# Performance work log

Measured on AMD Instinct MI355X. Metric: run time of the kernel, lower is better.

The kernel has to match this reference:

```python
import jax, jax.numpy as jnp
import numpy as np

B, N, T, D = 64, 76, 128, 128
AH, HEADS, DFF, FAH = 8, 4, 512, 128
DK = D // HEADS


def layer_norm(x, a, b, eps=1e-7):
    mean = x.mean(-1, keepdims=True)
    std = jnp.std(x, -1, ddof=1, keepdims=True)  # torch.std is unbiased
    return a * (x - mean) / (std + eps) + b


def setup_inputs() -> dict:
    key = jax.random.key(0)
    ks = jax.random.split(key, 32)
    w = lambda i, shape, s=0.05: (jax.random.normal(ks[i], shape, jnp.float32) * s)
    return {
        "H": jax.random.normal(ks[0], (B, N, T, D), jnp.float32),
        "mask": jax.random.randint(ks[1], (B, N, T), 0, 2).astype(jnp.float32),
        "feature_mask": jax.random.uniform(ks[2], (B, N), dtype=jnp.float32),
        # MissingAwareTemporalAttention params (shared across features)
        "Wt": w(3, (D, AH), 0.1), "Wx": w(4, (D, AH), 0.1),
        "rate": jnp.array([0.8], jnp.float32),
        "obs_bias": jnp.float32(0.5), "miss_bias": jnp.float32(0.0),
        # MultiHeadedAttention params (weights stored [in,out])
        "Wq": w(5, (D, D)), "bq": jnp.zeros(D, jnp.float32),
        "Wk": w(6, (D, D)), "bk": jnp.zeros(D, jnp.float32),
        "Wv": w(7, (D, D)), "bv": jnp.zeros(D, jnp.float32),
        "Wo": w(8, (D, D)), "bo": jnp.zeros(D, jnp.float32),
        # SublayerConnection LayerNorms
        "ln1_a": jnp.ones(D, jnp.float32), "ln1_b": jnp.zeros(D, jnp.float32),
        "ln2_a": jnp.ones(D, jnp.float32), "ln2_b": jnp.zeros(D, jnp.float32),
        # PositionwiseFeedForward
        "w1": w(9, (D, DFF)), "b1": jnp.zeros(DFF, jnp.float32),
        "w2": w(10, (DFF, D)), "b2": jnp.zeros(D, jnp.float32),
        # FinalAttentionQKV ('mul')
        "fWq": w(11, (D, FAH)), "fbq": jnp.zeros(FAH, jnp.float32),
        "fWk": w(12, (D, FAH)), "fbk": jnp.zeros(FAH, jnp.float32),
        "fWv": w(13, (D, FAH)), "fbv": jnp.zeros(FAH, jnp.float32),
        "mask_scale": jnp.float32(1.0),
    }


def concare_forward(H, mask, feature_mask, Wt, Wx, rate, obs_bias, miss_bias,
                    Wq, bq, Wk, bk, Wv, bv, Wo, bo, ln1_a, ln1_b, ln2_a, ln2_b,
                    w1, b1, w2, b2, fWq, fbq, fWk, fbk, fWv, fbv, mask_scale):
    # ---- MissingAwareTemporalAttention per feature (vectorized over N) ----
    q = jnp.einsum('bnd,da->bna', H[:, :, -1, :], Wt)           # [B,N,AH]
    k = jnp.einsum('bntd,da->bnta', H, Wx)                      # [B,N,T,AH]
    dot = jnp.einsum('bna,bnta->bnt', q, k)                     # [B,N,T]
    b_time = (jnp.arange(T - 1, -1, -1, dtype=jnp.float32) + 1.0)  # [T]
    sig = jax.nn.sigmoid(dot)
    denom = jax.nn.sigmoid(rate[0]) * (jnp.log(2.72 + (1.0 - sig)) * b_time)
    e = jax.nn.relu(sig / denom)
    e = e + jnp.where(mask > 0.5, obs_bias, miss_bias)
    a = jax.nn.softmax(e, axis=-1)                              # over T
    emb = jnp.einsum('bnt,bntd->bnd', a, H)                     # [B,N,D]

    # ---- SublayerConnection 1: pre-norm + MultiHeadedAttention + residual ----
    x0 = layer_norm(emb, ln1_a, ln1_b)
    qh = (x0 @ Wq + bq).reshape(B, N, HEADS, DK).transpose(0, 2, 1, 3)
    kh = (x0 @ Wk + bk).reshape(B, N, HEADS, DK).transpose(0, 2, 1, 3)
    vh = (x0 @ Wv + bv).reshape(B, N, HEADS, DK).transpose(0, 2, 1, 3)
    scores = jnp.einsum('bhqd,bhkd->bhqk', qh, kh) / np.sqrt(DK)
    p = jax.nn.softmax(scores, axis=-1)
    ctx = jnp.einsum('bhqk,bhkd->bhqd', p, vh).transpose(0, 2, 1, 3).reshape(B, N, D)
    mha = ctx @ Wo + bo                                          # [B,N,D]
    # DeCov regularizer over batch, per feature position
    feats = jnp.transpose(mha, (1, 2, 0))                        # [N,D,B]
    centered = feats - feats.mean(axis=2, keepdims=True)
    cov = jnp.einsum('ndb,neb->nde', centered, centered) / (B - 1)
    diag = jnp.einsum('ndd->nd', cov)
    decov = 0.5 * (jnp.sum(cov ** 2) - jnp.sum(diag ** 2))
    x = emb + mha

    # ---- SublayerConnection 2: pre-norm + FFN + residual ----
    x1 = layer_norm(x, ln2_a, ln2_b)
    ffn = jax.nn.relu(x1 @ w1 + b1) @ w2 + b2
    x = x + ffn                                                  # [B,N,D]

    # ---- FinalAttentionQKV ('mul') ----
    fq = x[:, -1, :] @ fWq + fbq                                 # [B,FAH]
    fk = x @ fWk + fbk                                           # [B,N,FAH]
    fv = x @ fWv + fbv                                           # [B,N,FAH]
    fe = jnp.einsum('bna,ba->bn', fk, fq)
    fe = fe + mask_scale * feature_mask
    alpha = jax.nn.softmax(fe, axis=1)                           # over N
    pooled = jnp.einsum('bn,bna->ba', alpha, fv)                 # [B,FAH]
    return pooled, decov


def reference(H, mask, feature_mask, Wt, Wx, rate, obs_bias, miss_bias,
              Wq, bq, Wk, bk, Wv, bv, Wo, bo, ln1_a, ln1_b, ln2_a, ln2_b,
              w1, b1, w2, b2, fWq, fbq, fWk, fbk, fWv, fbv, mask_scale):
    return concare_forward(H, mask, feature_mask, Wt, Wx, rate, obs_bias, miss_bias,
                           Wq, bq, Wk, bk, Wv, bv, Wo, bo, ln1_a, ln1_b, ln2_a, ln2_b,
                           w1, b1, w2, b2, fWq, fbq, fWk, fbk, fWv, fbv, mask_scale)
```

## Files before the change

kernel.cpp:

```cpp
#include <hip/hip_runtime.h>
#include <hip/hip_bf16.h>
#include <math.h>

#define BB 64
#define NN 76
#define TT 128
#define DD 128
#define AH 8
#define NHEADS 4
#define DFF 512
#define FAH 128
#define DK 32
#define BN (BB*NN)
#define ROWS 8
#define NBLK (BN/ROWS)

__device__ __forceinline__ void bar_lds() {
    asm volatile("s_waitcnt lgkmcnt(0)" ::: "memory");
    __builtin_amdgcn_s_barrier();
    __builtin_amdgcn_sched_barrier(0);
}

__global__ __launch_bounds__(512, 6) void k1_temporal(
    const float* __restrict__ H, const float* __restrict__ mask,
    const float* __restrict__ Wt, const float* __restrict__ Wx,
    const float* __restrict__ rate, const float* __restrict__ obs_bias,
    const float* __restrict__ miss_bias, float* __restrict__ emb)
{
    __shared__ __align__(16) float wqs[DD];
    __shared__ __align__(16) float dots[TT];
    __shared__ __align__(16) float as_[TT];
    __shared__ __align__(16) float parts[16][DD];
    __shared__ float qpart[2][AH];
    __shared__ float redmax[2];
    __shared__ float redsum[2];

    const int bid = blockIdx.x;
    const int tid = threadIdx.x;
    const size_t base = (size_t)bid * (TT*DD);

    float r127 = 0.f, maskv = 0.f;
    float4 wt0 = {0,0,0,0}, wt1 = {0,0,0,0}, wx0 = {0,0,0,0}, wx1 = {0,0,0,0};
    if (tid < DD) {
        r127 = H[base + (TT-1)*DD + tid];
        wt0 = *(const float4*)&Wt[tid*AH + 0];
        wt1 = *(const float4*)&Wt[tid*AH + 4];
        wx0 = *(const float4*)&Wx[tid*AH + 0];
        wx1 = *(const float4*)&Wx[tid*AH + 4];
        maskv = mask[(size_t)bid*TT + tid];
    }
    const float ratev = rate[0], obsv = obs_bias[0], missv = miss_bias[0];

    float4 h[8];
    const float4* Hg4 = (const float4*)(H + base);
    #pragma unroll
    for (int j = 0; j < 8; ++j) h[j] = Hg4[j*512 + tid];

    if (tid < DD) {
        float p[AH] = {r127*wt0.x, r127*wt0.y, r127*wt0.z, r127*wt0.w,
                       r127*wt1.x, r127*wt1.y, r127*wt1.z, r127*wt1.w};
        #pragma unroll
        for (int a = 0; a < AH; ++a) {
            float v = p[a];
            #pragma unroll
            for (int m = 1; m < 64; m <<= 1) v += __shfl_xor(v, m, 64);
            if ((tid & 63) == 0) qpart[tid >> 6][a] = v;
        }
    }
    bar_lds();
    if (tid < DD) {
        const float q0 = qpart[0][0]+qpart[1][0], q1 = qpart[0][1]+qpart[1][1];
        const float q2 = qpart[0][2]+qpart[1][2], q3 = qpart[0][3]+qpart[1][3];
        const float q4 = qpart[0][4]+qpart[1][4], q5 = qpart[0][5]+qpart[1][5];
        const float q6 = qpart[0][6]+qpart[1][6], q7 = qpart[0][7]+qpart[1][7];
        wqs[tid] = q0*wx0.x + q1*wx0.y + q2*wx0.z + q3*wx0.w
                 + q4*wx1.x + q5*wx1.y + q6*wx1.z + q7*wx1.w;
    }
    bar_lds();

    const int c = tid & 31, g = tid >> 5;
    const float4 wq4 = *(const float4*)&wqs[4*c];
    #pragma unroll
    for (int j = 0; j < 8; ++j) {
        float p = h[j].x*wq4.x + h[j].y*wq4.y + h[j].z*wq4.z + h[j].w*wq4.w;
        #pragma unroll
        for (int m = 1; m < 32; m <<= 1) p += __shfl_xor(p, m, 64);
        if (c == 0) dots[g + 16*j] = p;
    }
    bar_lds();

    const int lane = tid & 63, w = tid >> 6;
    float ev = -1e30f;
    if (tid < TT) {
        const float dot = dots[tid];
        const float sig = 1.f / (1.f + expf(-dot));
        const float sr  = 1.f / (1.f + expf(-ratev));
        const float bt  = (float)(TT - tid);
        const float denom = sr * (logf(2.72f + (1.f - sig)) * bt);
        float e = fmaxf(sig / denom, 0.f);
        e += (maskv > 0.5f) ? obsv : missv;
        ev = e;
        float vmax = ev;
        #pragma unroll
        for (int m = 1; m < 64; m <<= 1) vmax = fmaxf(vmax, __shfl_xor(vmax, m, 64));
        if (lane == 0) redmax[w] = vmax;
    }
    bar_lds();
    const float mx = fmaxf(redmax[0], redmax[1]);
    const float ex = (tid < TT) ? expf(ev - mx) : 0.f;
    if (tid < TT) {
        float vs = ex;
        #pragma unroll
        for (int m = 1; m < 64; m <<= 1) vs += __shfl_xor(vs, m, 64);
        if (lane == 0) redsum[w] = vs;
    }
    bar_lds();
    const float ssum = redsum[0] + redsum[1];
    if (tid < TT) as_[tid] = ex / ssum;
    bar_lds();

    float4 facc = make_float4(0.f, 0.f, 0.f, 0.f);
    #pragma unroll
    for (int j = 0; j < 8; ++j) {
        const float a = as_[g + 16*j];
        facc.x += a*h[j].x; facc.y += a*h[j].y;
        facc.z += a*h[j].z; facc.w += a*h[j].w;
    }
    *(float4*)&parts[g][4*c] = facc;
    bar_lds();
    if (tid < DD) {
        float acc = 0.f;
        #pragma unroll
        for (int gg = 0; gg < 16; ++gg) acc += parts[gg][tid];
        emb[(size_t)bid*DD + tid] = acc;
    }
}

__global__ __launch_bounds__(256) void k2a_ln_qkv(
    const float* __restrict__ emb,
    const float* __restrict__ ln_a, const float* __restrict__ ln_b,
    const float* __restrict__ Wq, const float* __restrict__ bq,
    const float* __restrict__ Wk, const float* __restrict__ bk,
    const float* __restrict__ Wv, const float* __restrict__ bv,
    float* __restrict__ qb, float* __restrict__ kb, float* __restrict__ vb)
{
    __shared__ float xs[ROWS][DD];
    const int tid = threadIdx.x;
    const int r0 = blockIdx.x * ROWS;

    for (int i = tid; i < ROWS*DD; i += 256) {
        const int r = i / DD, d = i % DD;
        xs[r][d] = emb[(size_t)(r0+r)*DD + d];
    }
    __syncthreads();

    {
        const int wv_ = tid >> 6, lane = tid & 63;
        for (int rr = 0; rr < 2; ++rr) {
            const int r = wv_*2 + rr;
            const float x0 = xs[r][lane], x1 = xs[r][lane+64];
            float s = x0 + x1;
            #pragma unroll
            for (int m = 1; m < 64; m <<= 1) s += __shfl_xor(s, m, 64);
            const float mean = s / (float)DD;
            const float d0 = x0 - mean, d1 = x1 - mean;
            float v = d0*d0 + d1*d1;
            #pragma unroll
            for (int m = 1; m < 64; m <<= 1) v += __shfl_xor(v, m, 64);
            const float inv = 1.f / (sqrtf(v / (float)(DD-1)) + 1e-7f);
            xs[r][lane]    = ln_a[lane]   * (d0*inv) + ln_b[lane];
            xs[r][lane+64] = ln_a[lane+64]* (d1*inv) + ln_b[lane+64];
        }
    }
    __syncthreads();

    const int j = tid & 127, half = tid >> 7, rbase = half*4;
    float aq[4] = {0,0,0,0}, ak[4] = {0,0,0,0}, av[4] = {0,0,0,0};
    for (int d = 0; d < DD; ++d) {
        const float wqv = Wq[d*DD+j], wkv = Wk[d*DD+j], wvv = Wv[d*DD+j];
        #pragma unroll
        for (int r = 0; r < 4; ++r) {
            const float xv = xs[rbase+r][d];
            aq[r] += xv*wqv; ak[r] += xv*wkv; av[r] += xv*wvv;
        }
    }
    const float bqv = bq[j], bkv = bk[j], bvv = bv[j];
    #pragma unroll
    for (int r = 0; r < 4; ++r) {
        const size_t o = (size_t)(r0 + rbase + r)*DD + j;
        qb[o] = aq[r]+bqv; kb[o] = ak[r]+bkv; vb[o] = av[r]+bvv;
    }
}

__global__ __launch_bounds__(128) void k2b_attn(
    const float* __restrict__ qb, const float* __restrict__ kb,
    const float* __restrict__ vb, float* __restrict__ ctx)
{
    __shared__ float Qs[NN][DK], Ks[NN][DK], Vs[NN][DK];
    __shared__ float Ps[NN][NN+1];
    const int b = blockIdx.x / NHEADS, h = blockIdx.x % NHEADS;
    const int tid = threadIdx.x;
    const int co = h*DK;

    for (int i = tid; i < NN*DK; i += 128) {
        const int r = i / DK, c = i % DK;
        const size_t o = (size_t)(b*NN + r)*DD + co + c;
        Qs[r][c] = qb[o]; Ks[r][c] = kb[o]; Vs[r][c] = vb[o];
    }
    __syncthreads();

    const float scale = 0.17677669529663687f;
    if (tid < NN) {
        float qr[DK];
        #pragma unroll
        for (int c = 0; c < DK; ++c) qr[c] = Qs[tid][c];
        float mx = -1e30f;
        for (int k = 0; k < NN; ++k) {
            float s = 0.f;
            #pragma unroll
            for (int c = 0; c < DK; ++c) s += qr[c]*Ks[k][c];
            s *= scale;
            Ps[tid][k] = s;
            mx = fmaxf(mx, s);
        }
        float sum = 0.f;
        for (int k = 0; k < NN; ++k) { const float e = expf(Ps[tid][k]-mx); Ps[tid][k] = e; sum += e; }
        const float inv = 1.f/sum;
        float acc[DK];
        #pragma unroll
        for (int c = 0; c < DK; ++c) acc[c] = 0.f;
        for (int k = 0; k < NN; ++k) {
            const float p = Ps[tid][k];
            #pragma unroll
            for (int c = 0; c < DK; ++c) acc[c] += p*Vs[k][c];
        }
        const size_t o = (size_t)(b*NN + tid)*DD + co;
        #pragma unroll
        for (int c = 0; c < DK; ++c) ctx[o+c] = acc[c]*inv;
    }
}

__global__ __launch_bounds__(256) void k23_proj_ffn(
    const float* __restrict__ ctx, const float* __restrict__ emb,
    const float* __restrict__ Wo, const float* __restrict__ bo,
    const float* __restrict__ ln_a, const float* __restrict__ ln_b,
    const float* __restrict__ w1, const float* __restrict__ b1,
    const float* __restrict__ w2, const float* __restrict__ b2,
    float* __restrict__ mha, float* __restrict__ x2)
{
    __shared__ float cs[ROWS][DD];
    __shared__ float xs[ROWS][DD];
    __shared__ float x1s[ROWS][DD];
    __shared__ float hs[ROWS][DFF];
    __shared__ float parts[2][ROWS][DD];
    const int tid = threadIdx.x;
    const int r0 = blockIdx.x * ROWS;

    for (int i = tid; i < ROWS*DD; i += 256) {
        const int r = i / DD, d = i % DD;
        cs[r][d] = ctx[(size_t)(r0+r)*DD + d];
    }
    __syncthreads();

    {
        const int j = tid & 127, half = tid >> 7, rbase = half*4;
        float acc[4] = {0,0,0,0};
        for (int d = 0; d < DD; ++d) {
            const float wv = Wo[d*DD+j];
            #pragma unroll
            for (int r = 0; r < 4; ++r) acc[r] += cs[rbase+r][d]*wv;
        }
        const float bov = bo[j];
        #pragma unroll
        for (int r = 0; r < 4; ++r) {
            const size_t o = (size_t)(r0+rbase+r)*DD + j;
            const float m = acc[r] + bov;
            mha[o] = m;
            xs[rbase+r][j] = emb[o] + m;
        }
    }
    __syncthreads();

    {
        const int wv_ = tid >> 6, lane = tid & 63;
        for (int rr = 0; rr < 2; ++rr) {
            const int r = wv_*2 + rr;
            const float v0 = xs[r][lane], v1 = xs[r][lane+64];
            float s = v0 + v1;
            #pragma unroll
            for (int m = 1; m < 64; m <<= 1) s += __shfl_xor(s, m, 64);
            const float mean = s / (float)DD;
            const float d0 = v0-mean, d1 = v1-mean;
            float vv = d0*d0 + d1*d1;
            #pragma unroll
            for (int m = 1; m < 64; m <<= 1) vv += __shfl_xor(vv, m, 64);
            const float inv = 1.f / (sqrtf(vv/(float)(DD-1)) + 1e-7f);
            x1s[r][lane]    = ln_a[lane]   * (d0*inv) + ln_b[lane];
            x1s[r][lane+64] = ln_a[lane+64]* (d1*inv) + ln_b[lane+64];
        }
    }
    __syncthreads();

    {
        float acc0[ROWS], acc1[ROWS];
        #pragma unroll
        for (int r = 0; r < ROWS; ++r) { acc0[r]=0.f; acc1[r]=0.f; }
        for (int d = 0; d < DD; ++d) {
            const float wv0 = w1[d*DFF + tid], wv1 = w1[d*DFF + tid + 256];
            #pragma unroll
            for (int r = 0; r < ROWS; ++r) {
                const float xv = x1s[r][d];
                acc0[r] += xv*wv0; acc1[r] += xv*wv1;
            }
        }
        const float b10 = b1[tid], b11 = b1[tid+256];
        #pragma unroll
        for (int r = 0; r < ROWS; ++r) {
            hs[r][tid]     = fmaxf(acc0[r]+b10, 0.f);
            hs[r][tid+256] = fmaxf(acc1[r]+b11, 0.f);
        }
    }
    __syncthreads();

    {
        const int j = tid & 127, half = tid >> 7;
        float acc[ROWS];
        #pragma unroll
        for (int r = 0; r < ROWS; ++r) acc[r] = 0.f;
        for (int k = half*256; k < half*256 + 256; ++k) {
            const float wv = w2[k*DD + j];
            #pragma unroll
            for (int r = 0; r < ROWS; ++r) acc[r] += hs[r][k]*wv;
        }
        #pragma unroll
        for (int r = 0; r < ROWS; ++r) parts[half][r][j] = acc[r];
        __syncthreads();
        if (half == 0) {
            const float b2v = b2[j];
            #pragma unroll
            for (int r = 0; r < ROWS; ++r) {
                const size_t o = (size_t)(r0+r)*DD + j;
                x2[o] = xs[r][j] + parts[0][r][j] + parts[1][r][j] + b2v;
            }
        }
    }
}

__global__ __launch_bounds__(256) void k_decov(
    const float* __restrict__ mha, float* __restrict__ partial)
{
    __shared__ float Cs[BB][DD];
    __shared__ float means[DD];
    __shared__ float reda[256];
    __shared__ float redb[256];
    const int n = blockIdx.x, dc = blockIdx.y;
    const int tid = threadIdx.x;
    for (int i = tid; i < BB*DD; i += 256) {
        const int bb = i / DD, d = i % DD;
        Cs[bb][d] = mha[((size_t)bb*NN + n)*DD + d];
    }
    __syncthreads();
    if (tid < DD) {
        float s = 0.f;
        for (int bb = 0; bb < BB; ++bb) s += Cs[bb][tid];
        means[tid] = s / (float)BB;
    }
    __syncthreads();
    if (tid < DD) {
        const float m = means[tid];
        for (int bb = 0; bb < BB; ++bb) Cs[bb][tid] -= m;
    }
    __syncthreads();
    float ss = 0.f, dd2 = 0.f;
    const float invB1 = 1.f/63.f;
    for (int qi = tid; qi < 1024; qi += 256) {
        const int d  = dc*32 + qi / 32;
        const int e4 = (qi % 32) * 4;
        float a0=0,a1=0,a2=0,a3=0;
        for (int bb = 0; bb < BB; ++bb) {
            const float cd = Cs[bb][d];
            const float4 ce = *(const float4*)&Cs[bb][e4];
            a0 += cd*ce.x; a1 += cd*ce.y; a2 += cd*ce.z; a3 += cd*ce.w;
        }
        a0*=invB1; a1*=invB1; a2*=invB1; a3*=invB1;
        ss += a0*a0+a1*a1+a2*a2+a3*a3;
        if (d >= e4 && d < e4+4) {
            const float c[4] = {a0,a1,a2,a3};
            const float cd = c[d-e4];
            dd2 += cd*cd;
        }
    }
    reda[tid] = ss; redb[tid] = dd2;
    __syncthreads();
    for (int s2 = 128; s2 >= 1; s2 >>= 1) {
        if (tid < s2) { reda[tid] += reda[tid+s2]; redb[tid] += redb[tid+s2]; }
        __syncthreads();
    }
    if (tid == 0) partial[n*4 + dc] = 0.5f*(reda[0] - redb[0]);
}

__global__ __launch_bounds__(128) void k4_final(
    const float* __restrict__ x, const float* __restrict__ feature_mask,
    const float* __restrict__ fWq, const float* __restrict__ fbq,
    const float* __restrict__ fWk, const float* __restrict__ fbk,
    const float* __restrict__ fWv, const float* __restrict__ fbv,
    const float* __restrict__ mask_scale, const float* __restrict__ decov_partial,
    float* __restrict__ out)
{
    __shared__ float Xs[NN][DD];
    __shared__ float fqs[DD], gs[DD], ys[DD];
    __shared__ float es[NN];
    __shared__ float sc[2];
    const int b = blockIdx.x;
    const int tid = threadIdx.x;
    for (int i = tid; i < NN*DD; i += 128) {
        const int r = i / DD, d = i % DD;
        Xs[r][d] = x[((size_t)b*NN + r)*DD + d];
    }
    __syncthreads();
    {
        float acc = 0.f;
        for (int d = 0; d < DD; ++d) acc += Xs[NN-1][d] * fWq[d*FAH + tid];
        fqs[tid] = acc + fbq[tid];
    }
    __syncthreads();
    {
        float acc = 0.f;
        for (int a = 0; a < FAH; ++a) acc += fWk[tid*FAH + a] * fqs[a];
        gs[tid] = acc;
    }
    if (tid == 0) {
        float acc = 0.f;
        for (int a = 0; a < FAH; ++a) acc += fbk[a]*fqs[a];
        sc[0] = acc;
    }
    __syncthreads();
    const float msc = mask_scale[0];
    if (tid < NN) {
        float acc = 0.f;
        for (int d = 0; d < DD; ++d) acc += Xs[tid][d]*gs[d];
        es[tid] = acc + sc[0] + msc * feature_mask[b*NN + tid];
    }
    __syncthreads();
    if (tid == 0) {
        float mx = -1e30f;
        for (int n2 = 0; n2 < NN; ++n2) mx = fmaxf(mx, es[n2]);
        float sum = 0.f;
        for (int n2 = 0; n2 < NN; ++n2) { const float e = expf(es[n2]-mx); es[n2] = e; sum += e; }
        sc[1] = 1.f/sum;
    }
    __syncthreads();
    {
        const float inv = sc[1];
        float acc = 0.f;
        for (int n2 = 0; n2 < NN; ++n2) acc += es[n2]*Xs[n2][tid];
        ys[tid] = acc * inv;
    }
    __syncthreads();
    {
        float acc = 0.f;
        for (int d = 0; d < DD; ++d) acc += ys[d]*fWv[d*FAH + tid];
        out[(size_t)b*FAH + tid] = acc + fbv[tid];
    }
    if (b == 0 && tid == 0) {
        float s = 0.f;
        for (int i = 0; i < NN*4; ++i) s += decov_partial[i];
        out[BB*FAH] = s;
    }
}

extern "C" void kernel_launch(void* const* d_in, const int* in_sizes, int n_in,
                              void* d_out, int out_size, void* d_ws, size_t ws_size,
                              hipStream_t stream) {
    const float* H    = (const float*)d_in[0];
    const float* mask = (const float*)d_in[1];
    const float* fm   = (const float*)d_in[2];
    const float* Wt   = (const float*)d_in[3];
    const float* Wx   = (const float*)d_in[4];
    const float* rate = (const float*)d_in[5];
    const float* obs_bias  = (const float*)d_in[6];
    const float* miss_bias = (const float*)d_in[7];
    const float* Wq = (const float*)d_in[8];   const float* bq = (const float*)d_in[9];
    const float* Wk = (const float*)d_in[10];  const float* bk = (const float*)d_in[11];
    const float* Wv = (const float*)d_in[12];  const float* bv = (const float*)d_in[13];
    const float* Wo = (const float*)d_in[14];  const float* bo = (const float*)d_in[15];
    const float* ln1a = (const float*)d_in[16]; const float* ln1b = (const float*)d_in[17];
    const float* ln2a = (const float*)d_in[18]; const float* ln2b = (const float*)d_in[19];
    const float* w1 = (const float*)d_in[20];  const float* b1 = (const float*)d_in[21];
    const float* w2 = (const float*)d_in[22];  const float* b2 = (const float*)d_in[23];
    const float* fWq = (const float*)d_in[24]; const float* fbq = (const float*)d_in[25];
    const float* fWk = (const float*)d_in[26]; const float* fbk = (const float*)d_in[27];
    const float* fWv = (const float*)d_in[28]; const float* fbv = (const float*)d_in[29];
    const float* mask_scale = (const float*)d_in[30];
    float* out = (float*)d_out;

    float* ws = (float*)d_ws;
    const size_t S = (size_t)BN*DD;
    float* emb = ws;
    float* qb  = ws + 1*S;
    float* kb  = ws + 2*S;
    float* vb  = ws + 3*S;
    float* ctx = ws + 4*S;
    float* mha = ws + 5*S;
    float* x2  = ws + 6*S;
    float* dpart = ws + 7*S;

    k1_temporal<<<BN, 512, 0, stream>>>(H, mask, Wt, Wx, rate, obs_bias, miss_bias, emb);
    k2a_ln_qkv<<<NBLK, 256, 0, stream>>>(emb, ln1a, ln1b, Wq, bq, Wk, bk, Wv, bv, qb, kb, vb);
    k2b_attn<<<BB*NHEADS, 128, 0, stream>>>(qb, kb, vb, ctx);
    k23_proj_ffn<<<NBLK, 256, 0, stream>>>(ctx, emb, Wo, bo, ln2a, ln2b, w1, b1, w2, b2, mha, x2);
    k_decov<<<dim3(NN, 4), 256, 0, stream>>>(mha, dpart);
    k4_final<<<BB, 128, 0, stream>>>(x2, fm, fWq, fbq, fWk, fbk, fWv, fbv, mask_scale, dpart, out);
}
```

Measured before the change: 181.3 us.

## Make temporal kernel persistent with double-buffered LDS DMA prefetch of H tiles

The temporal attention kernel becomes persistent: 256 blocks each loop over 19 (b,n) sequences instead of one block per sequence. Each 64KB H tile is copied straight into LDS with global_load_lds, double-buffered so the next tile loads while the current one is processed. This aims to hide HBM latency and cut launch and scheduling overhead. The cost is 128KB of LDS per block (one block per CU), a single tile of lookahead, and two redundant tile loads per block at the loop tail.

```diff
diff --git a/kernel.cpp b/kernel.cpp
--- a/kernel.cpp
+++ b/kernel.cpp
@@ -14,6 +14,8 @@
 #define BN (BB*NN)
 #define ROWS 8
 #define NBLK (BN/ROWS)
+#define K1BLK 256
+#define K1NT (BN/K1BLK)
 
 __device__ __forceinline__ void bar_lds() {
     asm volatile("s_waitcnt lgkmcnt(0)" ::: "memory");
@@ -21,12 +23,19 @@
     __builtin_amdgcn_sched_barrier(0);
 }
 
-__global__ __launch_bounds__(512, 6) void k1_temporal(
+__device__ __forceinline__ void dma16(const float* g, float* l) {
+    __builtin_amdgcn_global_load_lds(
+        (__attribute__((address_space(1))) void*)g,
+        (__attribute__((address_space(3))) void*)l, 16, 0, 0);
+}
+
+__global__ __launch_bounds__(512) void k1_temporal(
     const float* __restrict__ H, const float* __restrict__ mask,
     const float* __restrict__ Wt, const float* __restrict__ Wx,
     const float* __restrict__ rate, const float* __restrict__ obs_bias,
     const float* __restrict__ miss_bias, float* __restrict__ emb)
 {
+    __shared__ __align__(16) float buf[2][TT*DD];
     __shared__ __align__(16) float wqs[DD];
     __shared__ __align__(16) float dots[TT];
     __shared__ __align__(16) float as_[TT];
@@ -35,104 +44,137 @@
     __shared__ float redmax[2];
     __shared__ float redsum[2];
 
-    const int bid = blockIdx.x;
     const int tid = threadIdx.x;
-    const size_t base = (size_t)bid * (TT*DD);
-
-    float r127 = 0.f, maskv = 0.f;
+    const int lane = tid & 63, w = tid >> 6;
+    const int c = tid & 31, g = tid >> 5;
+    const int t0 = blockIdx.x * K1NT;
+
     float4 wt0 = {0,0,0,0}, wt1 = {0,0,0,0}, wx0 = {0,0,0,0}, wx1 = {0,0,0,0};
+    float mA = 0.f, mB = 0.f;
     if (tid < DD) {
-        r127 = H[base + (TT-1)*DD + tid];
         wt0 = *(const float4*)&Wt[tid*AH + 0];
         wt1 = *(const float4*)&Wt[tid*AH + 4];
         wx0 = *(const float4*)&Wx[tid*AH + 0];
         wx1 = *(const float4*)&Wx[tid*AH + 4];
-        maskv = mask[(size_t)bid*TT + tid];
-    }
-    const float ratev = rate[0], obsv = obs_bias[0], missv = miss_bias[0];
-
-    float4 h[8];
-    const float4* Hg4 = (const float4*)(H + base);
-    #pragma unroll
-    for (int j = 0; j < 8; ++j) h[j] = Hg4[j*512 + tid];
-
-    if (tid < DD) {
-        float p[AH] = {r127*wt0.x, r127*wt0.y, r127*wt0.z, r127*wt0.w,
-                       r127*wt1.x, r127*wt1.y, r127*wt1.z, r127*wt1.w};
-        #pragma unroll
-        for (int a = 0; a < AH; ++a) {
-            float v = p[a];
-            #pragma unroll
-            for (int m = 1; m < 64; m <<= 1) v += __shfl_xor(v, m, 64);
-            if ((tid & 63) == 0) qpart[tid >> 6][a] = v;
-        }
-    }
-    bar_lds();
-    if (tid < DD) {
-        const float q0 = qpart[0][0]+qpart[1][0], q1 = qpart[0][1]+qpart[1][1];
-        const float q2 = qpart[0][2]+qpart[1][2], q3 = qpart[0][3]+qpart[1][3];
-        const float q4 = qpart[0][4]+qpart[1][4], q5 = qpart[0][5]+qpart[1][5];
-        const float q6 = qpart[0][6]+qpart[1][6], q7 = qpart[0][7]+qpart[1][7];
-        wqs[tid] = q0*wx0.x + q1*wx0.y + q2*wx0.z + q3*wx0.w
-                 + q4*wx1.x + q5*wx1.y + q6*wx1.z + q7*wx1.w;
-    }
-    bar_lds();
-
-    const int c = tid & 31, g = tid >> 5;
-    const float4 wq4 = *(const float4*)&wqs[4*c];
-    #pragma unroll
-    for (int j = 0; j < 8; ++j) {
-        float p = h[j].x*wq4.x + h[j].y*wq4.y + h[j].z*wq4.z + h[j].w*wq4.w;
-        #pragma unroll
-        for (int m = 1; m < 32; m <<= 1) p += __shfl_xor(p, m, 64);
-        if (c == 0) dots[g + 16*j] = p;
-    }
-    bar_lds();
-
-    const int lane = tid & 63, w = tid >> 6;
-    float ev = -1e30f;
-    if (tid < TT) {
-        const float dot = dots[tid];
-        const float sig = 1.f / (1.f + expf(-dot));
-        const float sr  = 1.f / (1.f + expf(-ratev));
-        const float bt  = (float)(TT - tid);
-        const float denom = sr * (logf(2.72f + (1.f - sig)) * bt);
-        float e = fmaxf(sig / denom, 0.f);
-        e += (maskv > 0.5f) ? obsv : missv;
-        ev = e;
-        float vmax = ev;
-        #pragma unroll
-        for (int m = 1; m < 64; m <<= 1) vmax = fmaxf(vmax, __shfl_xor(vmax, m, 64));
-        if (lane == 0) redmax[w] = vmax;
-    }
-    bar_lds();
-    const float mx = fmaxf(redmax[0], redmax[1]);
-    const float ex = (tid < TT) ? expf(ev - mx) : 0.f;
-    if (tid < TT) {
-        float vs = ex;
-        #pragma unroll
-        for (int m = 1; m < 64; m <<= 1) vs += __shfl_xor(vs, m, 64);
-        if (lane == 0) redsum[w] = vs;
-    }
-    bar_lds();
-    const float ssum = redsum[0] + redsum[1];
-    if (tid < TT) as_[tid] = ex / ssum;
-    bar_lds();
-
-    float4 facc = make_float4(0.f, 0.f, 0.f, 0.f);
-    #pragma unroll
-    for (int j = 0; j < 8; ++j) {
-        const float a = as_[g + 16*j];
-        facc.x += a*h[j].x; facc.y += a*h[j].y;
-        facc.z += a*h[j].z; facc.w += a*h[j].w;
-    }
-    *(float4*)&parts[g][4*c] = facc;
-    bar_lds();
-    if (tid < DD) {
-        float acc = 0.f;
-        #pragma unroll
-        for (int gg = 0; gg < 16; ++gg) acc += parts[gg][tid];
-        emb[(size_t)bid*DD + tid] = acc;
+        mA = mask[(size_t)(t0+0)*TT + tid];
+        mB = mask[(size_t)(t0+1)*TT + tid];
+    }
+    const float sr   = 1.f / (1.f + expf(-rate[0]));
+    const float obsv = obs_bias[0], missv = miss_bias[0];
+
+    asm volatile("s_waitcnt vmcnt(0)" ::: "memory");
+    __syncthreads();
+
+    auto issue = [&](int t, int s) {
+        const float* gb = H + (size_t)t * (TT*DD);
+        float* lb = &buf[s][0];
+        #pragma unroll
+        for (int k = 0; k < 8; ++k) {
+            const int ch = w*8 + k;
+            dma16(gb + ch*256 + lane*4, lb + ch*256);
+        }
+    };
+
+    issue(t0 + 0, 0);
+    issue(t0 + 1, 1);
+
+    int cur = 0;
+    #pragma unroll 1
+    for (int i = 0; i < K1NT; ++i) {
+        asm volatile("s_waitcnt vmcnt(8)" ::: "memory");
+        __builtin_amdgcn_s_barrier();
+        __builtin_amdgcn_sched_barrier(0);
+
+        const float* Bf = &buf[cur][0];
+        const int t = t0 + i;
+        const float mv = cur ? mB : mA;
+
+        if (tid < DD) {
+            const float r127 = Bf[127*DD + tid];
+            float p[AH] = {r127*wt0.x, r127*wt0.y, r127*wt0.z, r127*wt0.w,
+                           r127*wt1.x, r127*wt1.y, r127*wt1.z, r127*wt1.w};
+            #pragma unroll
+            for (int a = 0; a < AH; ++a) {
+                float v = p[a];
+                #pragma unroll
+                for (int m = 1; m < 64; m <<= 1) v += __shfl_xor(v, m, 64);
+                if (lane == 0) qpart[w][a] = v;
+            }
+        }
+        bar_lds();
+        if (tid < DD) {
+            const float q0 = qpart[0][0]+qpart[1][0], q1 = qpart[0][1]+qpart[1][1];
+            const float q2 = qpart[0][2]+qpart[1][2], q3 = qpart[0][3]+qpart[1][3];
+            const float q4 = qpart[0][4]+qpart[1][4], q5 = qpart[0][5]+qpart[1][5];
+            const float q6 = qpart[0][6]+qpart[1][6], q7 = qpart[0][7]+qpart[1][7];
+            wqs[tid] = q0*wx0.x + q1*wx0.y + q2*wx0.z + q3*wx0.w
+                     + q4*wx1.x + q5*wx1.y + q6*wx1.z + q7*wx1.w;
+        }
+        bar_lds();
+
+        float4 h[8];
+        const float4 wq4 = *(const float4*)&wqs[4*c];
+        #pragma unroll
+        for (int j = 0; j < 8; ++j) {
+            h[j] = *(const float4*)&Bf[(g + 16*j)*DD + 4*c];
+            float p = h[j].x*wq4.x + h[j].y*wq4.y + h[j].z*wq4.z + h[j].w*wq4.w;
+            #pragma unroll
+            for (int m = 1; m < 32; m <<= 1) p += __shfl_xor(p, m, 64);
+            if (c == 0) dots[g + 16*j] = p;
+        }
+        bar_lds();
+
+        float ev = -1e30f;
+        if (tid < TT) {
+            const float dot = dots[tid];
+            const float sig = 1.f / (1.f + expf(-dot));
+            const float bt  = (float)(TT - tid);
+            const float denom = sr * (logf(2.72f + (1.f - sig)) * bt);
+            float e = fmaxf(sig / denom, 0.f);
+            e += (mv > 0.5f) ? obsv : missv;
+            ev = e;
+            float vmax = ev;
+            #pragma unroll
+            for (int m = 1; m < 64; m <<= 1) vmax = fmaxf(vmax, __shfl_xor(vmax, m, 64));
+            if (lane == 0) redmax[w] = vmax;
+        }
+        bar_lds();
+        const float mx = fmaxf(redmax[0], redmax[1]);
+        const float ex = (tid < TT) ? expf(ev - mx) : 0.f;
+        if (tid < TT) {
+            float vs = ex;
+            #pragma unroll
+            for (int m = 1; m < 64; m <<= 1) vs += __shfl_xor(vs, m, 64);
+            if (lane == 0) redsum[w] = vs;
+        }
+        bar_lds();
+        const float ssum = redsum[0] + redsum[1];
+        if (tid < TT) as_[tid] = ex / ssum;
+        bar_lds();
+
+        float4 facc = make_float4(0.f, 0.f, 0.f, 0.f);
+        #pragma unroll
+        for (int j = 0; j < 8; ++j) {
+            const float a = as_[g + 16*j];
+            facc.x += a*h[j].x; facc.y += a*h[j].y;
+            facc.z += a*h[j].z; facc.w += a*h[j].w;
+        }
+        *(float4*)&parts[g][4*c] = facc;
+        bar_lds();
+        if (tid < DD) {
+            float acc = 0.f;
+            #pragma unroll
+            for (int gg = 0; gg < 16; ++gg) acc += parts[gg][tid];
+            emb[(size_t)t*DD + tid] = acc;
+        }
+
+        const int tn = (i + 2 < K1NT) ? (t0 + i + 2) : t0;
+        if (tid < DD) {
+            const float mnew = mask[(size_t)tn*TT + tid];
+            if (cur) mB = mnew; else mA = mnew;
+        }
+        issue(tn, cur);
+        cur ^= 1;
     }
 }
 
@@ -505,7 +547,7 @@
     float* x2  = ws + 6*S;
     float* dpart = ws + 7*S;
 
-    k1_temporal<<<BN, 512, 0, stream>>>(H, mask, Wt, Wx, rate, obs_bias, miss_bias, emb);
+    k1_temporal<<<K1BLK, 512, 0, stream>>>(H, mask, Wt, Wx, rate, obs_bias, miss_bias, emb);
     k2a_ln_qkv<<<NBLK, 256, 0, stream>>>(emb, ln1a, ln1b, Wq, bq, Wk, bk, Wv, bv, qb, kb, vb);
     k2b_attn<<<BB*NHEADS, 128, 0, stream>>>(qb, kb, vb, ctx);
     k23_proj_ffn<<<NBLK, 256, 0, stream>>>(ctx, emb, Wo, bo, ln2a, ln2b, w1, b1, w2, b2, mha, x2);
```

Result: slower. 251.1 us (+38.5%).
